# Performance work log

Hardware: AMD Instinct MI355X
Metric: run time of the kernel (lower is better)

## Reference

```python
import jax, jax.numpy as jnp
import numpy as np

D_MODEL = 1024
NHEAD = 16
HEAD_DIM = D_MODEL // NHEAD
B, S = 2, 2048


def setup_inputs() -> dict:
    key = jax.random.key(0)
    ks = jax.random.split(key, 10)
    inp = {
        "q": jax.random.normal(ks[0], (B, S, D_MODEL), jnp.float32),
        "k": jax.random.normal(ks[1], (B, S, D_MODEL), jnp.float32),
        "v": jax.random.normal(ks[2], (B, S, D_MODEL), jnp.float32),
        # parameters (torch used randn init; scale down for numerical sanity is NOT
        # done to stay faithful to randn, but we use unit normal like the module)
        "q_proj_weight": jax.random.normal(ks[3], (D_MODEL, D_MODEL), jnp.float32) * 0.02,
        "k_proj_weight": jax.random.normal(ks[4], (D_MODEL, D_MODEL), jnp.float32) * 0.02,
        "v_proj_weight": jax.random.normal(ks[5], (D_MODEL, D_MODEL), jnp.float32) * 0.02,
        "out_proj_weight": jax.random.normal(ks[6], (D_MODEL, D_MODEL), jnp.float32) * 0.02,
        "gate_weight": jax.random.normal(ks[7], (D_MODEL, D_MODEL), jnp.float32) * 0.02,
        "gate_bias": jax.random.normal(ks[8], (D_MODEL,), jnp.float32) * 0.02,
        "scale_weight": jax.random.normal(ks[9], (NHEAD, HEAD_DIM), jnp.float32) * 0.02,
    }
    return inp


def reference(q, k, v, q_proj_weight, k_proj_weight, v_proj_weight,
              out_proj_weight, gate_weight, gate_bias, scale_weight):
    b, s, _ = q.shape
    # projections: x @ W (note: NOT transposed, matching torch.matmul(x, W))
    qp = jnp.matmul(q, q_proj_weight)
    kp = jnp.matmul(k, k_proj_weight)
    vp = jnp.matmul(v, v_proj_weight)
    # [B,H,S,Dh]
    qh = qp.reshape(b, s, NHEAD, HEAD_DIM).transpose(0, 2, 1, 3)
    kh = kp.reshape(b, s, NHEAD, HEAD_DIM).transpose(0, 2, 1, 3)
    vh = vp.reshape(b, s, NHEAD, HEAD_DIM).transpose(0, 2, 1, 3)
    inv_sqrt = 1.0 / jnp.sqrt(jnp.asarray(HEAD_DIM, qh.dtype))
    # [B,H,S,S]
    scores = jnp.einsum('bhsd,bhtd->bhst', qh, kh) * inv_sqrt
    # per-query sigmoid scale gate: [B,H,S]
    scale = jax.nn.sigmoid(jnp.einsum('bhsd,hd->bhs', qh, scale_weight)) * 2.0
    scores = scores * scale[..., None]
    attn = jax.nn.softmax(scores, axis=-1)
    out = jnp.einsum('bhst,bhtd->bhsd', attn, vh)  # [B,H,S,Dh]
    out = out.transpose(0, 2, 1, 3).reshape(b, s, D_MODEL)
    gate = jax.nn.sigmoid(jnp.matmul(out, gate_weight) + gate_bias)
    out = out * gate
    return jnp.matmul(out, out_proj_weight)
```

## Files before the change

kernel.cpp:

```cpp
#include <hip/hip_runtime.h>
#include <stdint.h>

typedef short          bf16x8_t __attribute__((ext_vector_type(8)));
typedef unsigned short u16x4_t  __attribute__((ext_vector_type(4)));
typedef unsigned short u16x8_t  __attribute__((ext_vector_type(8)));
typedef float          f32x4_t  __attribute__((ext_vector_type(4)));

#define AS1 __attribute__((address_space(1)))
#define AS3 __attribute__((address_space(3)))

static __device__ __forceinline__ unsigned short f2bf(float f) {
    union { float f; unsigned u; } v; v.f = f;
    unsigned r = v.u + 0x7FFFu + ((v.u >> 16) & 1u);
    return (unsigned short)(r >> 16);
}
static __device__ __forceinline__ float bf2f(unsigned short h) {
    union { unsigned u; float f; } v; v.u = ((unsigned)h) << 16;
    return v.f;
}
static __device__ __forceinline__ float bf2f_s(short s) { return bf2f((unsigned short)s); }

static __device__ __forceinline__ f32x4_t mfma16(bf16x8_t a, bf16x8_t b, f32x4_t c) {
    return __builtin_amdgcn_mfma_f32_16x16x32_bf16(a, b, c, 0, 0, 0);
}

static __device__ __forceinline__ float fexp2(float x) {
#if __has_builtin(__builtin_amdgcn_exp2f)
    return __builtin_amdgcn_exp2f(x);
#else
    return __exp2f(x);
#endif
}

static __device__ __forceinline__ unsigned cvtpk(float a, float b) {
    unsigned r;
    asm("v_cvt_pk_bf16_f32 %0, %1, %2" : "=v"(r) : "v"(a), "v"(b));
    return r;
}

static __device__ __forceinline__ void gload16(const unsigned short* g, unsigned short* l) {
    __builtin_amdgcn_global_load_lds(
        (const AS1 unsigned int*)(g),
        (AS3 unsigned int*)(uintptr_t)(l),
        16, 0, 0);
}

__global__ void conv3_bf16(const float* __restrict__ q, const float* __restrict__ k,
                           const float* __restrict__ v,
                           unsigned short* __restrict__ qb, unsigned short* __restrict__ kb,
                           unsigned short* __restrict__ vb)
{
    const int i = blockIdx.x * blockDim.x + threadIdx.x;
    const int which = i >> 20;
    const int r = i & 0xFFFFF;
    const float* s = which == 0 ? q : (which == 1 ? k : v);
    unsigned short* d = which == 0 ? qb : (which == 1 ? kb : vb);
    float4 f = ((const float4*)s)[r];
    u16x4_t o;
    o[0] = f2bf(f.x); o[1] = f2bf(f.y); o[2] = f2bf(f.z); o[3] = f2bf(f.w);
    ((u16x4_t*)d)[r] = o;
}

__global__ void transw5(const float* __restrict__ W0, const float* __restrict__ W1,
                        const float* __restrict__ W2, const float* __restrict__ W3,
                        const float* __restrict__ W4,
                        unsigned short* __restrict__ T0, unsigned short* __restrict__ T1,
                        unsigned short* __restrict__ T2, unsigned short* __restrict__ T3,
                        unsigned short* __restrict__ T4)
{
    __shared__ float tile[32][33];
    const int which = blockIdx.x >> 10;
    const int bb = blockIdx.x & 1023;
    const float* W = which == 0 ? W0 : which == 1 ? W1 : which == 2 ? W2 : which == 3 ? W3 : W4;
    unsigned short* WT = which == 0 ? T0 : which == 1 ? T1 : which == 2 ? T2 : which == 3 ? T3 : T4;
    const int bx = bb & 31, by = bb >> 5;
    const int k0 = by * 32, n0 = bx * 32;
    const int c = threadIdx.x & 31, r0 = threadIdx.x >> 5;
    #pragma unroll
    for (int i = 0; i < 4; i++) {
        int r = r0 + i * 8;
        tile[r][c] = W[(size_t)(k0 + r) * 1024 + n0 + c];
    }
    __syncthreads();
    #pragma unroll
    for (int i = 0; i < 4; i++) {
        int r = r0 + i * 8;
        WT[(size_t)(n0 + r) * 1024 + k0 + c] = f2bf(tile[c][r]);
    }
}

__global__ __launch_bounds__(256, 2)
void gemm128(const unsigned short* __restrict__ A, size_t sA,
             const unsigned short* __restrict__ BT, size_t sB,
             unsigned short* __restrict__ C, size_t sC,
             unsigned short* __restrict__ vTout)
{
    __shared__ unsigned short Al[128 * 32];
    __shared__ unsigned short Bl[128 * 32];
    const int t = threadIdx.x;
    const int w = t >> 6, lane = t & 63, g = lane >> 4, lr = lane & 15;
    const int nwg = gridDim.x;
    const int bid = (blockIdx.x & 7) * (nwg >> 3) + (blockIdx.x >> 3);
    const int bat = bid >> 8;
    const int rem = bid & 255;
    const int bm = rem >> 3, bn = rem & 7;
    const int m0 = bm << 7, n0 = bn << 7;
    const int wm = (w >> 1) << 6, wn = (w & 1) << 6;
    const int K = 1024, N = 1024;

    f32x4_t acc[4][4];
    #pragma unroll
    for (int i = 0; i < 4; i++)
        #pragma unroll
        for (int j = 0; j < 4; j++) acc[i][j] = (f32x4_t){0.f, 0.f, 0.f, 0.f};

    const int srow = t >> 2, sk = (t & 3) << 3;
    const unsigned short* ga = A  + (size_t)bat * sA + (size_t)(m0 + srow) * K + sk;
    const unsigned short* gb = BT + (size_t)bat * sB + (size_t)(n0 + srow) * K + sk;
    unsigned short* Ad = Al + w * 512;
    unsigned short* Bd = Bl + w * 512;
    const size_t half = (size_t)64 * K;

    for (int kt = 0; kt < K; kt += 32) {
        gload16(ga,        Ad);
        gload16(ga + half, Ad + 2048);
        gload16(gb,        Bd);
        gload16(gb + half, Bd + 2048);
        ga += 32; gb += 32;
        __syncthreads();
        bf16x8_t af[4], bfr[4];
        #pragma unroll
        for (int i = 0; i < 4; i++) af[i]  = *(const bf16x8_t*)&Al[(wm + i * 16 + lr) * 32 + g * 8];
        #pragma unroll
        for (int j = 0; j < 4; j++) bfr[j] = *(const bf16x8_t*)&Bl[(wn + j * 16 + lr) * 32 + g * 8];
        __builtin_amdgcn_s_setprio(1);
        #pragma unroll
        for (int i = 0; i < 4; i++)
            #pragma unroll
            for (int j = 0; j < 4; j++)
                acc[i][j] = mfma16(af[i], bfr[j], acc[i][j]);
        __builtin_amdgcn_s_setprio(0);
        __syncthreads();
    }

    #pragma unroll
    for (int i = 0; i < 4; i++) {
        #pragma unroll
        for (int j = 0; j < 4; j++) {
            #pragma unroll
            for (int r = 0; r < 4; r++) {
                const int row = m0 + wm + i * 16 + g * 4 + r;
                const int col = n0 + wn + j * 16 + lr;
                const float v = acc[i][j][r];
                if (bat < 2) {
                    C[(size_t)bat * sC + (size_t)row * N + col] = f2bf(v);
                } else {
                    const int bb = row >> 11, s = row & 2047;
                    const int hh = col >> 6, dd = col & 63;
                    vTout[(((size_t)(bb * 16 + hh) << 6) + dd) * 2048 + s] = f2bf(v);
                }
            }
        }
    }
}

__global__ __launch_bounds__(256, 4)
void gemm64(const unsigned short* __restrict__ A,
            const unsigned short* __restrict__ BT,
            void* __restrict__ C,
            const float* __restrict__ bias,
            const unsigned short* __restrict__ mul,
            int M, int N, int K, int epi)
{
    __shared__ unsigned short Al[64 * 32];
    __shared__ unsigned short Bl[128 * 32];
    const int t = threadIdx.x;
    const int w = t >> 6, lane = t & 63, g = lane >> 4, lr = lane & 15;
    const int nwg = gridDim.x;
    const int bid = (blockIdx.x & 7) * (nwg >> 3) + (blockIdx.x >> 3);
    const int nn = N >> 7;
    const int bm = bid / nn, bn = bid - (bid / nn) * nn;
    const int m0 = bm << 6, n0 = bn << 7;

    f32x4_t acc[4][2];
    #pragma unroll
    for (int i = 0; i < 4; i++)
        #pragma unroll
        for (int j = 0; j < 2; j++) acc[i][j] = (f32x4_t){0.f, 0.f, 0.f, 0.f};

    const unsigned short* ga = A + (size_t)(m0 + (t >> 2)) * K + ((t & 3) << 3);
    const int jb0 = w * 128 + lane, jb1 = jb0 + 64;
    const unsigned short* gb0 = BT + (size_t)(n0 + (jb0 >> 2)) * K + ((jb0 & 3) << 3);
    const unsigned short* gb1 = BT + (size_t)(n0 + (jb1 >> 2)) * K + ((jb1 & 3) << 3);
    unsigned short* Ad  = Al + w * 512;
    unsigned short* Bd0 = Bl + (size_t)(w * 128) * 8;
    unsigned short* Bd1 = Bl + (size_t)(w * 128 + 64) * 8;

    for (int kt = 0; kt < K; kt += 32) {
        gload16(ga, Ad);
        gload16(gb0, Bd0);
        gload16(gb1, Bd1);
        ga += 32; gb0 += 32; gb1 += 32;
        __syncthreads();
        bf16x8_t af[4], bfr[2];
        #pragma unroll
        for (int i = 0; i < 4; i++) af[i]  = *(const bf16x8_t*)&Al[(i * 16 + lr) * 32 + g * 8];
        #pragma unroll
        for (int j = 0; j < 2; j++) bfr[j] = *(const bf16x8_t*)&Bl[(w * 32 + j * 16 + lr) * 32 + g * 8];
        __builtin_amdgcn_s_setprio(1);
        #pragma unroll
        for (int i = 0; i < 4; i++)
            #pragma unroll
            for (int j = 0; j < 2; j++)
                acc[i][j] = mfma16(af[i], bfr[j], acc[i][j]);
        __builtin_amdgcn_s_setprio(0);
        __syncthreads();
    }

    #pragma unroll
    for (int i = 0; i < 4; i++) {
        #pragma unroll
        for (int j = 0; j < 2; j++) {
            #pragma unroll
            for (int r = 0; r < 4; r++) {
                const int row = m0 + i * 16 + g * 4 + r;
                const int col = n0 + w * 32 + j * 16 + lr;
                const float v = acc[i][j][r];
                if (epi == 1) {
                    const float pre = v + bias[col];
                    const float gt = 1.f / (1.f + __expf(-pre));
                    const size_t idx = (size_t)row * N + col;
                    ((unsigned short*)C)[idx] = f2bf(bf2f(mul[idx]) * gt);
                } else {
                    ((float*)C)[(size_t)row * N + col] = v;
                }
            }
        }
    }
}

__global__ __launch_bounds__(256, 4)
void attn_fwd(const unsigned short* __restrict__ Qp,
              const unsigned short* __restrict__ Kp,
              const unsigned short* __restrict__ VT,
              const float* __restrict__ sw,
              unsigned short* __restrict__ O)
{
    __shared__ unsigned short Kl[2][4096];
    __shared__ unsigned short Vl[2][4096];
    __shared__ unsigned short Pl[4][1024];

    const int t = threadIdx.x;
    const int w = t >> 6, lane = t & 63;
    const int g = lane >> 4, lr = lane & 15;
    const int sw8 = lr & 7;
    const int bid = (blockIdx.x & 7) * 128 + (blockIdx.x >> 3);
    const int qt = bid & 31, h = (bid >> 5) & 15, b = bid >> 9;
    const int s0 = qt * 64 + w * 16;

    const size_t qrow = ((size_t)b * 2048 + s0 + lr) * 1024 + h * 64;
    bf16x8_t qf0 = *(const bf16x8_t*)&Qp[qrow + g * 8];
    bf16x8_t qf1 = *(const bf16x8_t*)&Qp[qrow + 32 + g * 8];
    const float* swh = sw + h * 64;
    float dot = 0.f;
    #pragma unroll
    for (int j = 0; j < 8; j++)
        dot += bf2f_s(qf0[j]) * swh[g * 8 + j] + bf2f_s(qf1[j]) * swh[32 + g * 8 + j];
    dot += __shfl_xor(dot, 16);
    dot += __shfl_xor(dot, 32);
    const float qsc = 0.36067376f / (1.f + __expf(-dot));
    #pragma unroll
    for (int j = 0; j < 8; j++) {
        qf0[j] = (short)f2bf(bf2f_s(qf0[j]) * qsc);
        qf1[j] = (short)f2bf(bf2f_s(qf1[j]) * qsc);
    }

    f32x4_t acc[4];
    #pragma unroll
    for (int db = 0; db < 4; db++) acc[db] = (f32x4_t){0.f, 0.f, 0.f, 0.f};
    float lsum = 0.f;

    const unsigned short* kbase = Kp + ((size_t)b * 2048) * 1024 + h * 64;
    const unsigned short* vtb   = VT + ((size_t)(b * 16 + h) * 64) * 2048;

#define STAGE(buf, kb)                                                          \
    { _Pragma("unroll")                                                         \
      for (int p = 0; p < 2; p++) {                                             \
          const int j = w * 128 + p * 64 + lane;                                \
          const int row = j >> 3, cc = j & 7;                                   \
          const int cs = (cc ^ (row & 7)) << 3;                                 \
          gload16(kbase + (size_t)((kb) + row) * 1024 + cs,                     \
                  &Kl[buf][(w * 128 + p * 64) * 8]);                            \
          gload16(vtb + (size_t)row * 2048 + (kb) + cs,                         \
                  &Vl[buf][(w * 128 + p * 64) * 8]);                            \
      } }

    STAGE(0, 0)
    __syncthreads();

    for (int ti = 0; ti < 32; ti++) {
        const int cur = ti & 1;
        if (ti < 31) STAGE(cur ^ 1, (ti + 1) * 64)

        const unsigned short* Kc = Kl[cur];
        const unsigned short* Vc = Vl[cur];
        unsigned short* Pw = Pl[w];

        f32x4_t st[4];
        #pragma unroll
        for (int kt = 0; kt < 4; kt++) st[kt] = (f32x4_t){0.f, 0.f, 0.f, 0.f};
        __builtin_amdgcn_s_setprio(1);
        #pragma unroll
        for (int kt = 0; kt < 4; kt++) {
            bf16x8_t ka0 = *(const bf16x8_t*)&Kc[(16 * kt + lr) * 64 + ((g ^ sw8) << 3)];
            st[kt] = mfma16(ka0, qf0, st[kt]);
            bf16x8_t ka1 = *(const bf16x8_t*)&Kc[(16 * kt + lr) * 64 + (((4 + g) ^ sw8) << 3)];
            st[kt] = mfma16(ka1, qf1, st[kt]);
        }
        __builtin_amdgcn_s_setprio(0);

        #pragma unroll
        for (int kt = 0; kt < 4; kt++) {
            const float e0 = fexp2(st[kt][0]);
            const float e1 = fexp2(st[kt][1]);
            const float e2 = fexp2(st[kt][2]);
            const float e3 = fexp2(st[kt][3]);
            lsum += (e0 + e1) + (e2 + e3);
            uint2 pw;
            pw.x = cvtpk(e0, e1);
            pw.y = cvtpk(e2, e3);
            const int cc = 2 * kt + (g >> 1);
            *(uint2*)&Pw[lr * 64 + ((cc ^ sw8) << 3) + ((g & 1) << 2)] = pw;
        }

        __builtin_amdgcn_s_setprio(1);
        #pragma unroll
        for (int kk = 0; kk < 2; kk++) {
            const bf16x8_t pf = *(const bf16x8_t*)&Pw[lr * 64 + (((4 * kk + g) ^ sw8) << 3)];
            #pragma unroll
            for (int db = 0; db < 4; db++) {
                const bf16x8_t vf =
                    *(const bf16x8_t*)&Vc[(db * 16 + lr) * 64 + (((4 * kk + g) ^ sw8) << 3)];
                acc[db] = mfma16(pf, vf, acc[db]);
            }
        }
        __builtin_amdgcn_s_setprio(0);
        __syncthreads();
    }
#undef STAGE

    lsum += __shfl_xor(lsum, 16);
    lsum += __shfl_xor(lsum, 32);
    const float inv = 1.f / lsum;
    const float i0 = __shfl(inv, 4 * g + 0);
    const float i1 = __shfl(inv, 4 * g + 1);
    const float i2 = __shfl(inv, 4 * g + 2);
    const float i3 = __shfl(inv, 4 * g + 3);
    const size_t ob = ((size_t)b * 2048 + s0) * 1024 + h * 64;
    #pragma unroll
    for (int db = 0; db < 4; db++) {
        O[ob + (size_t)(4 * g + 0) * 1024 + db * 16 + lr] = f2bf(acc[db][0] * i0);
        O[ob + (size_t)(4 * g + 1) * 1024 + db * 16 + lr] = f2bf(acc[db][1] * i1);
        O[ob + (size_t)(4 * g + 2) * 1024 + db * 16 + lr] = f2bf(acc[db][2] * i2);
        O[ob + (size_t)(4 * g + 3) * 1024 + db * 16 + lr] = f2bf(acc[db][3] * i3);
    }
}

extern "C" void kernel_launch(void* const* d_in, const int* in_sizes, int n_in,
                              void* d_out, int out_size, void* d_ws, size_t ws_size,
                              hipStream_t stream) {
    const float* q  = (const float*)d_in[0];
    const float* k  = (const float*)d_in[1];
    const float* v  = (const float*)d_in[2];
    const float* Wq = (const float*)d_in[3];
    const float* Wk = (const float*)d_in[4];
    const float* Wv = (const float*)d_in[5];
    const float* Wo = (const float*)d_in[6];
    const float* Wg = (const float*)d_in[7];
    const float* gbias = (const float*)d_in[8];
    const float* sw = (const float*)d_in[9];

    char* ws = (char*)d_ws;
    const size_t MB = 1024 * 1024;
    unsigned short* qb    = (unsigned short*)(ws + 0 * MB);
    unsigned short* kb    = (unsigned short*)(ws + 8 * MB);
    unsigned short* vb    = (unsigned short*)(ws + 16 * MB);
    unsigned short* WqT   = (unsigned short*)(ws + 24 * MB);
    unsigned short* WkT   = (unsigned short*)(ws + 26 * MB);
    unsigned short* WvT   = (unsigned short*)(ws + 28 * MB);
    unsigned short* WgT   = (unsigned short*)(ws + 30 * MB);
    unsigned short* WoT   = (unsigned short*)(ws + 32 * MB);
    unsigned short* qp    = (unsigned short*)(ws + 34 * MB);
    unsigned short* kp    = (unsigned short*)(ws + 42 * MB);
    unsigned short* vT    = (unsigned short*)(ws + 58 * MB);
    unsigned short* ao    = (unsigned short*)(ws + 66 * MB);
    unsigned short* gated = (unsigned short*)(ws + 74 * MB);

    const int TB = 256;

    conv3_bf16<<<12288, TB, 0, stream>>>(q, k, v, qb, kb, vb);
    transw5<<<5120, TB, 0, stream>>>(Wq, Wk, Wv, Wg, Wo, WqT, WkT, WvT, WgT, WoT);

    gemm128<<<768, TB, 0, stream>>>(qb, (size_t)4194304, WqT, (size_t)1048576,
                                    qp, (size_t)4194304, vT);

    attn_fwd<<<1024, TB, 0, stream>>>(qp, kp, vT, sw, ao);

    gemm64<<<512, TB, 0, stream>>>(ao, WgT, gated, gbias, ao, 4096, 1024, 1024, 1);
    gemm64<<<512, TB, 0, stream>>>(gated, WoT, d_out, nullptr, nullptr, 4096, 1024, 1024, 2);
}
```

Before: 265.6 us.

## Merge prep kernels, stage V-transpose epilogue via LDS, unroll attention loop by two

Folds the fp32-to-bf16 conversion and the weight-transpose kernels into one launch, which removes a kernel launch and the gap between them. The gemm128 V-projection epilogue now goes through an LDS tile so that the transposed V is written with 16-byte contiguous stores instead of scattered 2-byte stores. The attention loop is unrolled by two with fixed buffer indices and precomputed, pointer-incremented global addresses to cut index arithmetic. In exchange gemm128 uses about 17KB more LDS, which may reduce occupancy, and the epilogue adds extra barriers.

After: 248.2 us. 6.5% less time.

```diff
diff --git a/kernel.cpp b/kernel.cpp
--- a/kernel.cpp
+++ b/kernel.cpp
@@ -45,32 +45,33 @@
         16, 0, 0);
 }
 
-__global__ void conv3_bf16(const float* __restrict__ q, const float* __restrict__ k,
-                           const float* __restrict__ v,
-                           unsigned short* __restrict__ qb, unsigned short* __restrict__ kb,
-                           unsigned short* __restrict__ vb)
+__global__ void prep(const float* __restrict__ q, const float* __restrict__ k,
+                     const float* __restrict__ v,
+                     unsigned short* __restrict__ qb, unsigned short* __restrict__ kb,
+                     unsigned short* __restrict__ vb,
+                     const float* __restrict__ W0, const float* __restrict__ W1,
+                     const float* __restrict__ W2, const float* __restrict__ W3,
+                     const float* __restrict__ W4,
+                     unsigned short* __restrict__ T0, unsigned short* __restrict__ T1,
+                     unsigned short* __restrict__ T2, unsigned short* __restrict__ T3,
+                     unsigned short* __restrict__ T4)
 {
-    const int i = blockIdx.x * blockDim.x + threadIdx.x;
-    const int which = i >> 20;
-    const int r = i & 0xFFFFF;
-    const float* s = which == 0 ? q : (which == 1 ? k : v);
-    unsigned short* d = which == 0 ? qb : (which == 1 ? kb : vb);
-    float4 f = ((const float4*)s)[r];
-    u16x4_t o;
-    o[0] = f2bf(f.x); o[1] = f2bf(f.y); o[2] = f2bf(f.z); o[3] = f2bf(f.w);
-    ((u16x4_t*)d)[r] = o;
-}
-
-__global__ void transw5(const float* __restrict__ W0, const float* __restrict__ W1,
-                        const float* __restrict__ W2, const float* __restrict__ W3,
-                        const float* __restrict__ W4,
-                        unsigned short* __restrict__ T0, unsigned short* __restrict__ T1,
-                        unsigned short* __restrict__ T2, unsigned short* __restrict__ T3,
-                        unsigned short* __restrict__ T4)
-{
+    if (blockIdx.x < 12288) {
+        const int i = blockIdx.x * blockDim.x + threadIdx.x;
+        const int which = i >> 20;
+        const int r = i & 0xFFFFF;
+        const float* s = which == 0 ? q : (which == 1 ? k : v);
+        unsigned short* d = which == 0 ? qb : (which == 1 ? kb : vb);
+        float4 f = ((const float4*)s)[r];
+        u16x4_t o;
+        o[0] = f2bf(f.x); o[1] = f2bf(f.y); o[2] = f2bf(f.z); o[3] = f2bf(f.w);
+        ((u16x4_t*)d)[r] = o;
+        return;
+    }
     __shared__ float tile[32][33];
-    const int which = blockIdx.x >> 10;
-    const int bb = blockIdx.x & 1023;
+    const int bidw = blockIdx.x - 12288;
+    const int which = bidw >> 10;
+    const int bb = bidw & 1023;
     const float* W = which == 0 ? W0 : which == 1 ? W1 : which == 2 ? W2 : which == 3 ? W3 : W4;
     unsigned short* WT = which == 0 ? T0 : which == 1 ? T1 : which == 2 ? T2 : which == 3 ? T3 : T4;
     const int bx = bb & 31, by = bb >> 5;
@@ -97,6 +98,7 @@
 {
     __shared__ unsigned short Al[128 * 32];
     __shared__ unsigned short Bl[128 * 32];
+    __shared__ unsigned short Tl[64 * 136];
     const int t = threadIdx.x;
     const int w = t >> 6, lane = t & 63, g = lane >> 4, lr = lane & 15;
     const int nwg = gridDim.x;
@@ -143,23 +145,47 @@
         __syncthreads();
     }
 
-    #pragma unroll
-    for (int i = 0; i < 4; i++) {
-        #pragma unroll
-        for (int j = 0; j < 4; j++) {
+    if (bat < 2) {
+        #pragma unroll
+        for (int i = 0; i < 4; i++) {
             #pragma unroll
-            for (int r = 0; r < 4; r++) {
-                const int row = m0 + wm + i * 16 + g * 4 + r;
-                const int col = n0 + wn + j * 16 + lr;
-                const float v = acc[i][j][r];
-                if (bat < 2) {
-                    C[(size_t)bat * sC + (size_t)row * N + col] = f2bf(v);
-                } else {
-                    const int bb = row >> 11, s = row & 2047;
-                    const int hh = col >> 6, dd = col & 63;
-                    vTout[(((size_t)(bb * 16 + hh) << 6) + dd) * 2048 + s] = f2bf(v);
+            for (int j = 0; j < 4; j++) {
+                #pragma unroll
+                for (int r = 0; r < 4; r++) {
+                    const int row = m0 + wm + i * 16 + g * 4 + r;
+                    const int col = n0 + wn + j * 16 + lr;
+                    C[(size_t)bat * sC + (size_t)row * N + col] = f2bf(acc[i][j][r]);
                 }
             }
+        }
+    } else {
+        const int cc = t >> 2, seg = t & 3;
+        #pragma unroll
+        for (int p = 0; p < 2; p++) {
+            if ((w & 1) == p) {
+                #pragma unroll
+                for (int i = 0; i < 4; i++)
+                    #pragma unroll
+                    for (int j = 0; j < 4; j++)
+                        #pragma unroll
+                        for (int r = 0; r < 4; r++)
+                            Tl[(j * 16 + lr) * 136 + wm + i * 16 + g * 4 + r] =
+                                f2bf(acc[i][j][r]);
+            }
+            __syncthreads();
+            {
+                const int col = n0 + p * 64 + cc;
+                const int hh = col >> 6, dd = col & 63;
+                const int bb = m0 >> 11;
+                const int sb = (m0 & 2047) + seg * 32;
+                unsigned short* dst =
+                    vTout + (((size_t)(bb * 16 + hh) << 6) + dd) * 2048 + sb;
+                const unsigned short* srcl = Tl + cc * 136 + seg * 32;
+                #pragma unroll
+                for (int m = 0; m < 4; m++)
+                    *(u16x8_t*)(dst + m * 8) = *(const u16x8_t*)(srcl + m * 8);
+            }
+            if (p == 0) __syncthreads();
         }
     }
 }
@@ -283,71 +309,81 @@
     const unsigned short* kbase = Kp + ((size_t)b * 2048) * 1024 + h * 64;
     const unsigned short* vtb   = VT + ((size_t)(b * 16 + h) * 64) * 2048;
 
-#define STAGE(buf, kb)                                                          \
-    { _Pragma("unroll")                                                         \
-      for (int p = 0; p < 2; p++) {                                             \
-          const int j = w * 128 + p * 64 + lane;                                \
-          const int row = j >> 3, cc = j & 7;                                   \
-          const int cs = (cc ^ (row & 7)) << 3;                                 \
-          gload16(kbase + (size_t)((kb) + row) * 1024 + cs,                     \
-                  &Kl[buf][(w * 128 + p * 64) * 8]);                            \
-          gload16(vtb + (size_t)row * 2048 + (kb) + cs,                         \
-                  &Vl[buf][(w * 128 + p * 64) * 8]);                            \
-      } }
-
-    STAGE(0, 0)
+    const int jj0 = w * 128 + lane, jj1 = jj0 + 64;
+    const int r0_ = jj0 >> 3, c0_ = ((jj0 & 7) ^ (r0_ & 7)) << 3;
+    const int r1_ = jj1 >> 3, c1_ = ((jj1 & 7) ^ (r1_ & 7)) << 3;
+    const unsigned short* kq0 = kbase + (size_t)r0_ * 1024 + c0_;
+    const unsigned short* kq1 = kbase + (size_t)r1_ * 1024 + c1_;
+    const unsigned short* vq0 = vtb + (size_t)r0_ * 2048 + c0_;
+    const unsigned short* vq1 = vtb + (size_t)r1_ * 2048 + c1_;
+    unsigned short* kd0 = &Kl[0][w * 1024];
+    unsigned short* vd0 = &Vl[0][w * 1024];
+
+#define STAGE(buf)                                                              \
+    gload16(kq0, kd0 + (buf) * 4096);                                           \
+    gload16(kq1, kd0 + (buf) * 4096 + 512);                                     \
+    gload16(vq0, vd0 + (buf) * 4096);                                           \
+    gload16(vq1, vd0 + (buf) * 4096 + 512);                                     \
+    kq0 += 65536; kq1 += 65536; vq0 += 64; vq1 += 64;
+
+#define COMPUTE(cur)                                                            \
+    {                                                                           \
+        const unsigned short* Kc = Kl[cur];                                     \
+        const unsigned short* Vc = Vl[cur];                                     \
+        unsigned short* Pw = Pl[w];                                             \
+        f32x4_t st[4];                                                          \
+        _Pragma("unroll")                                                       \
+        for (int kt = 0; kt < 4; kt++) st[kt] = (f32x4_t){0.f, 0.f, 0.f, 0.f};  \
+        __builtin_amdgcn_s_setprio(1);                                          \
+        _Pragma("unroll")                                                       \
+        for (int kt = 0; kt < 4; kt++) {                                        \
+            bf16x8_t ka0 = *(const bf16x8_t*)&Kc[(16 * kt + lr) * 64 + ((g ^ sw8) << 3)]; \
+            st[kt] = mfma16(ka0, qf0, st[kt]);                                  \
+            bf16x8_t ka1 = *(const bf16x8_t*)&Kc[(16 * kt + lr) * 64 + (((4 + g) ^ sw8) << 3)]; \
+            st[kt] = mfma16(ka1, qf1, st[kt]);                                  \
+        }                                                                       \
+        __builtin_amdgcn_s_setprio(0);                                          \
+        _Pragma("unroll")                                                       \
+        for (int kt = 0; kt < 4; kt++) {                                        \
+            const float e0 = fexp2(st[kt][0]);                                  \
+            const float e1 = fexp2(st[kt][1]);                                  \
+            const float e2 = fexp2(st[kt][2]);                                  \
+            const float e3 = fexp2(st[kt][3]);                                  \
+            lsum += (e0 + e1) + (e2 + e3);                                      \
+            uint2 pw2;                                                          \
+            pw2.x = cvtpk(e0, e1);                                              \
+            pw2.y = cvtpk(e2, e3);                                              \
+            const int ccx = 2 * kt + (g >> 1);                                  \
+            *(uint2*)&Pw[lr * 64 + ((ccx ^ sw8) << 3) + ((g & 1) << 2)] = pw2;  \
+        }                                                                       \
+        __builtin_amdgcn_s_setprio(1);                                          \
+        _Pragma("unroll")                                                       \
+        for (int kk = 0; kk < 2; kk++) {                                        \
+            const bf16x8_t pf = *(const bf16x8_t*)&Pw[lr * 64 + (((4 * kk + g) ^ sw8) << 3)]; \
+            _Pragma("unroll")                                                   \
+            for (int db = 0; db < 4; db++) {                                    \
+                const bf16x8_t vf =                                             \
+                    *(const bf16x8_t*)&Vc[(db * 16 + lr) * 64 + (((4 * kk + g) ^ sw8) << 3)]; \
+                acc[db] = mfma16(pf, vf, acc[db]);                              \
+            }                                                                   \
+        }                                                                       \
+        __builtin_amdgcn_s_setprio(0);                                          \
+    }
+
+    STAGE(0)
     __syncthreads();
 
-    for (int ti = 0; ti < 32; ti++) {
-        const int cur = ti & 1;
-        if (ti < 31) STAGE(cur ^ 1, (ti + 1) * 64)
-
-        const unsigned short* Kc = Kl[cur];
-        const unsigned short* Vc = Vl[cur];
-        unsigned short* Pw = Pl[w];
-
-        f32x4_t st[4];
-        #pragma unroll
-        for (int kt = 0; kt < 4; kt++) st[kt] = (f32x4_t){0.f, 0.f, 0.f, 0.f};
-        __builtin_amdgcn_s_setprio(1);
-        #pragma unroll
-        for (int kt = 0; kt < 4; kt++) {
-            bf16x8_t ka0 = *(const bf16x8_t*)&Kc[(16 * kt + lr) * 64 + ((g ^ sw8) << 3)];
-            st[kt] = mfma16(ka0, qf0, st[kt]);
-            bf16x8_t ka1 = *(const bf16x8_t*)&Kc[(16 * kt + lr) * 64 + (((4 + g) ^ sw8) << 3)];
-            st[kt] = mfma16(ka1, qf1, st[kt]);
-        }
-        __builtin_amdgcn_s_setprio(0);
-
-        #pragma unroll
-        for (int kt = 0; kt < 4; kt++) {
-            const float e0 = fexp2(st[kt][0]);
-            const float e1 = fexp2(st[kt][1]);
-            const float e2 = fexp2(st[kt][2]);
-            const float e3 = fexp2(st[kt][3]);
-            lsum += (e0 + e1) + (e2 + e3);
-            uint2 pw;
-            pw.x = cvtpk(e0, e1);
-            pw.y = cvtpk(e2, e3);
-            const int cc = 2 * kt + (g >> 1);
-            *(uint2*)&Pw[lr * 64 + ((cc ^ sw8) << 3) + ((g & 1) << 2)] = pw;
-        }
-
-        __builtin_amdgcn_s_setprio(1);
-        #pragma unroll
-        for (int kk = 0; kk < 2; kk++) {
-            const bf16x8_t pf = *(const bf16x8_t*)&Pw[lr * 64 + (((4 * kk + g) ^ sw8) << 3)];
-            #pragma unroll
-            for (int db = 0; db < 4; db++) {
-                const bf16x8_t vf =
-                    *(const bf16x8_t*)&Vc[(db * 16 + lr) * 64 + (((4 * kk + g) ^ sw8) << 3)];
-                acc[db] = mfma16(pf, vf, acc[db]);
-            }
-        }
-        __builtin_amdgcn_s_setprio(0);
+    #pragma unroll 1
+    for (int ti = 0; ti < 32; ti += 2) {
+        STAGE(1)
+        COMPUTE(0)
+        __syncthreads();
+        if (ti < 30) { STAGE(0) }
+        COMPUTE(1)
         __syncthreads();
     }
 #undef STAGE
+#undef COMPUTE
 
     lsum += __shfl_xor(lsum, 16);
     lsum += __shfl_xor(lsum, 32);
@@ -398,8 +434,8 @@
 
     const int TB = 256;
 
-    conv3_bf16<<<12288, TB, 0, stream>>>(q, k, v, qb, kb, vb);
-    transw5<<<5120, TB, 0, stream>>>(Wq, Wk, Wv, Wg, Wo, WqT, WkT, WvT, WgT, WoT);
+    prep<<<17408, TB, 0, stream>>>(q, k, v, qb, kb, vb,
+                                   Wq, Wk, Wv, Wg, Wo, WqT, WkT, WvT, WgT, WoT);
 
     gemm128<<<768, TB, 0, stream>>>(qb, (size_t)4194304, WqT, (size_t)1048576,
                                     qp, (size_t)4194304, vT);
```
